# Kernel tuning notes

Measured on AMD Instinct MI355X. Metric: run time of the kernel, lower is better.

The kernel has to match this reference:

```python
import jax, jax.numpy as jnp
import numpy as np

N = 10000
E = 330000
B = 8
F_IN = 128
UNITS = 32
H1 = 4  # gat1 heads, concat -> 128
H2 = 1  # gat2 heads, average/no-concat -> 32


def setup_inputs() -> dict:
    key = jax.random.key(0)
    ks = jax.random.split(key, 12)
    x = jax.random.normal(ks[0], (B, N, F_IN), dtype=jnp.float32)
    # edges: random src/dst plus self loops appended (as in build())
    src = jax.random.randint(ks[1], (E,), 0, N, dtype=jnp.int32)
    dst = jax.random.randint(ks[2], (E,), 0, N, dtype=jnp.int32)
    loops = jnp.arange(N, dtype=jnp.int32)
    edge_src = jnp.concatenate([src, loops])
    edge_dst = jnp.concatenate([dst, loops])
    s = 0.05
    # GAT layer 1: F_IN -> UNITS per head, H1 heads
    W1 = jax.random.normal(ks[3], (F_IN, H1, UNITS), dtype=jnp.float32) * s
    a1_src = jax.random.normal(ks[4], (H1, UNITS), dtype=jnp.float32) * s
    a1_dst = jax.random.normal(ks[5], (H1, UNITS), dtype=jnp.float32) * s
    b1 = jnp.zeros((H1 * UNITS,), dtype=jnp.float32)
    # GAT layer 2: H1*UNITS -> UNITS, 1 head
    W2 = jax.random.normal(ks[6], (H1 * UNITS, H2, UNITS), dtype=jnp.float32) * s
    a2_src = jax.random.normal(ks[7], (H2, UNITS), dtype=jnp.float32) * s
    a2_dst = jax.random.normal(ks[8], (H2, UNITS), dtype=jnp.float32) * s
    b2 = jnp.zeros((UNITS,), dtype=jnp.float32)
    return {"x": x, "edge_src": edge_src, "edge_dst": edge_dst,
            "W1": W1, "a1_src": a1_src, "a1_dst": a1_dst, "b1": b1,
            "W2": W2, "a2_src": a2_src, "a2_dst": a2_dst, "b2": b2}


def gat_conv(x, edge_src, edge_dst, W, a_src, a_dst, b, concat):
    # x: [B, N, F]; W: [F, H, U]
    Bn, Nn, _ = x.shape
    H, U = W.shape[1], W.shape[2]
    h = jnp.einsum('bnf,fhu->bnhu', x, W)  # [B,N,H,U]
    # per-node attention logits split into src/dst parts (GATv1 style)
    e_src = jnp.einsum('bnhu,hu->bnh', h, a_src)  # [B,N,H]
    e_dst = jnp.einsum('bnhu,hu->bnh', h, a_dst)
    # gather along edges; edge e: src -> dst, aggregate at dst
    logits = e_src[:, edge_src, :] + e_dst[:, edge_dst, :]  # [B,E,H]
    logits = jax.nn.leaky_relu(logits, 0.2)
    # segment softmax over incoming edges of each dst node
    seg_max = jax.ops.segment_max(jnp.moveaxis(logits, 1, 0), edge_dst,
                                  num_segments=Nn)  # [N,B,H]
    seg_max = jnp.where(jnp.isfinite(seg_max), seg_max, 0.0)
    expv = jnp.exp(jnp.moveaxis(logits, 1, 0) - seg_max[edge_dst])  # [E,B,H]
    denom = jax.ops.segment_sum(expv, edge_dst, num_segments=Nn)  # [N,B,H]
    alpha = expv / (denom[edge_dst] + 1e-9)  # [E,B,H]
    # weighted scatter-add of source features
    msg = jnp.moveaxis(h, 1, 0)[edge_src] * alpha[..., None]  # [E,B,H,U]
    out = jax.ops.segment_sum(msg, edge_dst, num_segments=Nn)  # [N,B,H,U]
    out = jnp.moveaxis(out, 0, 1)  # [B,N,H,U]
    if concat:
        out = out.reshape(Bn, Nn, H * U)
    else:
        out = out.mean(axis=2)
    return out + b


def reference(x, edge_src, edge_dst, W1, a1_src, a1_dst, b1, W2, a2_src, a2_dst, b2):
    h1 = gat_conv(x, edge_src, edge_dst, W1, a1_src, a1_dst, b1, concat=True)
    h1 = jax.nn.relu(h1)
    out = gat_conv(h1, edge_src, edge_dst, W2, a2_src, a2_dst, b2, concat=False)
    return out
```

## Files before the change

kernel.cpp:

```cpp
#include <hip/hip_runtime.h>
#include <hip/hip_fp16.h>

#define N_NODES 10000
#define BATCH 8
#define FIN 128
#define UNITS 32
#define NH1 4
#define MAXDEG 128

#define WAVE_FENCE() asm volatile("s_waitcnt lgkmcnt(0)" ::: "memory")

#define FMA_MIX_LO(acc, u, a) \
    asm("v_fma_mix_f32 %0, %1, %2, %0 op_sel:[0,0,0] op_sel_hi:[1,0,0]" \
        : "+v"(acc) : "v"(u), "v"(a))
#define FMA_MIX_HI(acc, u, a) \
    asm("v_fma_mix_f32 %0, %1, %2, %0 op_sel:[1,0,0] op_sel_hi:[1,0,0]" \
        : "+v"(acc) : "v"(u), "v"(a))

typedef _Float16 half8 __attribute__((ext_vector_type(8)));
typedef float f32x4 __attribute__((ext_vector_type(4)));

__global__ void prep_kernel(const float* __restrict__ W1, const float* __restrict__ a1s,
                            const float* __restrict__ a1d, const float* __restrict__ W2,
                            const float* __restrict__ a2s, const float* __restrict__ a2d,
                            __half* __restrict__ Wt1, __half* __restrict__ Wt2) {
    int t = blockIdx.x * blockDim.x + threadIdx.x;
    const int N1 = 144 * 128;
    if (t < N1) {
        int c = t >> 7, k = t & 127;
        float v = 0.f;
        if (c < 128) v = W1[k * 128 + c];
        else if (c < 132) {
            int h = c - 128;
            for (int u = 0; u < 32; ++u) v += W1[k * 128 + h * 32 + u] * a1s[h * 32 + u];
        } else if (c < 136) {
            int h = c - 132;
            for (int u = 0; u < 32; ++u) v += W1[k * 128 + h * 32 + u] * a1d[h * 32 + u];
        }
        Wt1[t] = __float2half(v);
    } else if (t < N1 + 48 * 128) {
        int q = t - N1;
        int c = q >> 7, k = q & 127;
        float v = 0.f;
        if (c < 32) v = W2[k * 32 + c];
        else if (c == 32) { for (int u = 0; u < 32; ++u) v += W2[k * 32 + u] * a2s[u]; }
        else if (c == 33) { for (int u = 0; u < 32; ++u) v += W2[k * 32 + u] * a2d[u]; }
        Wt2[q] = __float2half(v);
    }
}

template<typename XT, int NTILES, int HTILES, int ES>
__global__ __launch_bounds__(256)
void gemm_mfma(const XT* __restrict__ X, const __half* __restrict__ Wt,
               __half* __restrict__ Hout, float* __restrict__ es,
               float* __restrict__ ed, int rows) {
    constexpr int K = 128;
    constexpr int HCOLS = HTILES * 16;
    constexpr int PAD = 136;
    __shared__ _Float16 Wl[NTILES * 16][PAD];
    const int tid = threadIdx.x;
    for (int idx = tid; idx < NTILES * 16 * K / 8; idx += 256) {
        int r = idx >> 4, kq = idx & 15;
        *(half8*)&Wl[r][kq * 8] = *(const half8*)(Wt + r * K + kq * 8);
    }
    __syncthreads();
    const int w = tid >> 6, lane = tid & 63;
    const int row16 = blockIdx.x * 64 + w * 16;
    const int arow = row16 + (lane & 15);
    const int cl = lane & 15;
    f32x4 acc[NTILES] = {};
    #pragma unroll
    for (int kb = 0; kb < 4; ++kb) {
        int kbase = kb * 32 + ((lane >> 4) << 3);
        half8 a;
        if constexpr (sizeof(XT) == 4) {
            const float* xp = (const float*)X + (size_t)arow * K + kbase;
            float4 v0 = *(const float4*)xp;
            float4 v1 = *(const float4*)(xp + 4);
            a[0] = v0.x; a[1] = v0.y; a[2] = v0.z; a[3] = v0.w;
            a[4] = v1.x; a[5] = v1.y; a[6] = v1.z; a[7] = v1.w;
        } else {
            a = *(const half8*)((const _Float16*)X + (size_t)arow * K + kbase);
        }
        #pragma unroll
        for (int t = 0; t < NTILES; ++t) {
            half8 b = *(const half8*)&Wl[t * 16 + cl][kbase];
            acc[t] = __builtin_amdgcn_mfma_f32_16x16x32_f16(a, b, acc[t], 0, 0, 0);
        }
    }
    const int rbase = row16 + ((lane >> 4) << 2);
    #pragma unroll
    for (int t = 0; t < HTILES; ++t) {
        #pragma unroll
        for (int i = 0; i < 4; ++i)
            Hout[(size_t)(rbase + i) * HCOLS + t * 16 + cl] = __float2half(acc[t][i]);
    }
    {
        f32x4 lg = acc[HTILES];
        if (cl < ES) {
            #pragma unroll
            for (int i = 0; i < 4; ++i) es[(size_t)(rbase + i) * ES + cl] = lg[i];
        } else if (cl < 2 * ES) {
            #pragma unroll
            for (int i = 0; i < 4; ++i) ed[(size_t)(rbase + i) * ES + (cl - ES)] = lg[i];
        }
    }
}

__global__ void build_kernel(const int* __restrict__ esrc, const int* __restrict__ edst,
                             int* __restrict__ deg, int* __restrict__ colPad, int E) {
    int e = blockIdx.x * blockDim.x + threadIdx.x;
    if (e >= E) return;
    int d = edst[e];
    int pos = atomicAdd(&deg[d], 1);
    colPad[(d << 7) + pos] = esrc[e];
}

__global__ __launch_bounds__(512)
void agg1_kernel(const int* __restrict__ deg, const int* __restrict__ colPad,
                 const float* __restrict__ es, const float* __restrict__ ed,
                 const __half* __restrict__ Hf, const float* __restrict__ bias,
                 __half* __restrict__ outH) {
    __shared__ float evS[8][MAXDEG][4];
    __shared__ int colS[8][MAXDEG];
    int blk = blockIdx.x;
    int b = blk & 7;
    int grp = blk >> 3;
    int w = threadIdx.x >> 6;
    int d = grp * 8 + w;
    int lane = threadIdx.x & 63;
    int eg = lane >> 4;
    int c8 = lane & 15;
    int head = c8 >> 2;
    int n = deg[d];
    const int* colp = colPad + (d << 7);
    size_t brow = (size_t)b * N_NODES;
    size_t drow = brow + d;
    float4 ed4 = ((const float4*)ed)[drow];
    float dx = 0.f, dy = 0.f, dz = 0.f, dw = 0.f;
    #pragma unroll
    for (int rep = 0; rep < 2; ++rep) {
        int i = lane + rep * 64;
        if (i < n) {
            int s = colp[i];
            colS[w][i] = s;
            float4 e4 = ((const float4*)es)[brow + s];
            float l, a0, a1, a2, a3;
            l = e4.x + ed4.x; l = l > 0.f ? l : 0.2f * l; a0 = __expf(l); dx += a0;
            l = e4.y + ed4.y; l = l > 0.f ? l : 0.2f * l; a1 = __expf(l); dy += a1;
            l = e4.z + ed4.z; l = l > 0.f ? l : 0.2f * l; a2 = __expf(l); dz += a2;
            l = e4.w + ed4.w; l = l > 0.f ? l : 0.2f * l; a3 = __expf(l); dw += a3;
            *(float4*)&evS[w][i][0] = make_float4(a0, a1, a2, a3);
        }
    }
    WAVE_FENCE();
    float acc[8] = {};
    const __half* hbase = Hf + (brow << 7) + (c8 << 3);
    int n16 = n & ~15;
    for (int t = 0; t < n16; t += 16) {
        int t0 = t + eg, t1 = t0 + 4, t2 = t0 + 8, t3 = t0 + 12;
        float a0 = evS[w][t0][head], a1 = evS[w][t1][head];
        float a2 = evS[w][t2][head], a3 = evS[w][t3][head];
        int s0 = colS[w][t0], s1 = colS[w][t1], s2 = colS[w][t2], s3 = colS[w][t3];
        float4 r0 = *(const float4*)(hbase + ((size_t)s0 << 7));
        float4 r1 = *(const float4*)(hbase + ((size_t)s1 << 7));
        float4 r2 = *(const float4*)(hbase + ((size_t)s2 << 7));
        float4 r3 = *(const float4*)(hbase + ((size_t)s3 << 7));
        const unsigned* u0 = (const unsigned*)&r0;
        const unsigned* u1 = (const unsigned*)&r1;
        const unsigned* u2 = (const unsigned*)&r2;
        const unsigned* u3 = (const unsigned*)&r3;
        #pragma unroll
        for (int j = 0; j < 4; ++j) {
            FMA_MIX_LO(acc[2 * j],     u0[j], a0);
            FMA_MIX_HI(acc[2 * j + 1], u0[j], a0);
        }
        #pragma unroll
        for (int j = 0; j < 4; ++j) {
            FMA_MIX_LO(acc[2 * j],     u1[j], a1);
            FMA_MIX_HI(acc[2 * j + 1], u1[j], a1);
        }
        #pragma unroll
        for (int j = 0; j < 4; ++j) {
            FMA_MIX_LO(acc[2 * j],     u2[j], a2);
            FMA_MIX_HI(acc[2 * j + 1], u2[j], a2);
        }
        #pragma unroll
        for (int j = 0; j < 4; ++j) {
            FMA_MIX_LO(acc[2 * j],     u3[j], a3);
            FMA_MIX_HI(acc[2 * j + 1], u3[j], a3);
        }
    }
    for (int t = n16; t < n; t += 4) {
        int myt = t + eg;
        int tt = myt < n ? myt : 0;
        float a = evS[w][tt][head]; if (myt >= n) a = 0.f;
        int s = colS[w][tt];
        float4 r = *(const float4*)(hbase + ((size_t)s << 7));
        const unsigned* u = (const unsigned*)&r;
        #pragma unroll
        for (int j = 0; j < 4; ++j) {
            FMA_MIX_LO(acc[2 * j],     u[j], a);
            FMA_MIX_HI(acc[2 * j + 1], u[j], a);
        }
    }
    #pragma unroll
    for (int off = 32; off; off >>= 1) {
        dx += __shfl_xor(dx, off);
        dy += __shfl_xor(dy, off);
        dz += __shfl_xor(dz, off);
        dw += __shfl_xor(dw, off);
    }
    float ix = 1.f / (dx + 1e-9f);
    float iy = 1.f / (dy + 1e-9f);
    float iz = 1.f / (dz + 1e-9f);
    float iw = 1.f / (dw + 1e-9f);
    float inv = (head & 2) ? ((head & 1) ? iw : iz) : ((head & 1) ? iy : ix);
    #pragma unroll
    for (int j = 0; j < 8; ++j) {
        acc[j] += __shfl_xor(acc[j], 16);
        acc[j] += __shfl_xor(acc[j], 32);
    }
    if (eg == 0) {
        float4 b0 = *(const float4*)(bias + 8 * c8);
        float4 b1 = *(const float4*)(bias + 8 * c8 + 4);
        float vals[8];
        vals[0] = fmaxf(acc[0] * inv + b0.x, 0.f);
        vals[1] = fmaxf(acc[1] * inv + b0.y, 0.f);
        vals[2] = fmaxf(acc[2] * inv + b0.z, 0.f);
        vals[3] = fmaxf(acc[3] * inv + b0.w, 0.f);
        vals[4] = fmaxf(acc[4] * inv + b1.x, 0.f);
        vals[5] = fmaxf(acc[5] * inv + b1.y, 0.f);
        vals[6] = fmaxf(acc[6] * inv + b1.z, 0.f);
        vals[7] = fmaxf(acc[7] * inv + b1.w, 0.f);
        __half2 o[4];
        #pragma unroll
        for (int j = 0; j < 4; ++j) o[j] = __floats2half2_rn(vals[2 * j], vals[2 * j + 1]);
        *(float4*)(outH + drow * 128 + c8 * 8) = *(float4*)o;
    }
}

__global__ __launch_bounds__(512)
void agg2_kernel(const int* __restrict__ deg, const int* __restrict__ colPad,
                 const float* __restrict__ es, const float* __restrict__ ed,
                 const __half* __restrict__ Hf, const float* __restrict__ bias,
                 float* __restrict__ outF) {
    __shared__ float evS[8][MAXDEG];
    __shared__ int colS[8][MAXDEG];
    int blk = blockIdx.x;
    int b = blk & 7;
    int grp = blk >> 3;
    int w = threadIdx.x >> 6;
    int d = grp * 8 + w;
    int lane = threadIdx.x & 63;
    int eg = lane >> 2;
    int c8 = lane & 3;
    int n = deg[d];
    const int* colp = colPad + (d << 7);
    size_t brow = (size_t)b * N_NODES;
    size_t drow = brow + d;
    float edv = ed[drow];
    float den = 0.f;
    #pragma unroll
    for (int rep = 0; rep < 2; ++rep) {
        int i = lane + rep * 64;
        if (i < n) {
            int s = colp[i];
            colS[w][i] = s;
            float l = es[brow + s] + edv;
            l = l > 0.f ? l : 0.2f * l;
            float ev = __expf(l);
            den += ev;
            evS[w][i] = ev;
        }
    }
    WAVE_FENCE();
    float acc[8] = {};
    const __half* hbase = Hf + (brow << 5) + (c8 << 3);
    int n32 = n & ~31;
    for (int t = 0; t < n32; t += 32) {
        int t0 = t + eg, t1 = t0 + 16;
        float a0 = evS[w][t0];
        float a1 = evS[w][t1];
        int s0 = colS[w][t0];
        int s1 = colS[w][t1];
        float4 r0 = *(const float4*)(hbase + ((size_t)s0 << 5));
        float4 r1 = *(const float4*)(hbase + ((size_t)s1 << 5));
        const unsigned* u0 = (const unsigned*)&r0;
        const unsigned* u1 = (const unsigned*)&r1;
        #pragma unroll
        for (int j = 0; j < 4; ++j) {
            FMA_MIX_LO(acc[2 * j],     u0[j], a0);
            FMA_MIX_HI(acc[2 * j + 1], u0[j], a0);
        }
        #pragma unroll
        for (int j = 0; j < 4; ++j) {
            FMA_MIX_LO(acc[2 * j],     u1[j], a1);
            FMA_MIX_HI(acc[2 * j + 1], u1[j], a1);
        }
    }
    for (int t = n32; t < n; t += 16) {
        int myt = t + eg;
        int tt = myt < n ? myt : 0;
        float a = evS[w][tt]; if (myt >= n) a = 0.f;
        int s = colS[w][tt];
        float4 r = *(const float4*)(hbase + ((size_t)s << 5));
        const unsigned* u = (const unsigned*)&r;
        #pragma unroll
        for (int j = 0; j < 4; ++j) {
            FMA_MIX_LO(acc[2 * j],     u[j], a);
            FMA_MIX_HI(acc[2 * j + 1], u[j], a);
        }
    }
    #pragma unroll
    for (int off = 32; off; off >>= 1) den += __shfl_xor(den, off);
    float inv = 1.f / (den + 1e-9f);
    #pragma unroll
    for (int j = 0; j < 8; ++j) {
        acc[j] += __shfl_xor(acc[j], 4);
        acc[j] += __shfl_xor(acc[j], 8);
        acc[j] += __shfl_xor(acc[j], 16);
        acc[j] += __shfl_xor(acc[j], 32);
    }
    if (eg == 0) {
        float4 b0 = *(const float4*)(bias + 8 * c8);
        float4 b1 = *(const float4*)(bias + 8 * c8 + 4);
        float4 o0, o1;
        o0.x = acc[0] * inv + b0.x;
        o0.y = acc[1] * inv + b0.y;
        o0.z = acc[2] * inv + b0.z;
        o0.w = acc[3] * inv + b0.w;
        o1.x = acc[4] * inv + b1.x;
        o1.y = acc[5] * inv + b1.y;
        o1.z = acc[6] * inv + b1.z;
        o1.w = acc[7] * inv + b1.w;
        float* op = outF + drow * 32 + 8 * c8;
        *(float4*)op = o0;
        *(float4*)(op + 4) = o1;
    }
}

extern "C" void kernel_launch(void* const* d_in, const int* in_sizes, int n_in,
                              void* d_out, int out_size, void* d_ws, size_t ws_size,
                              hipStream_t stream) {
    const float* x    = (const float*)d_in[0];
    const int*   esrc = (const int*)d_in[1];
    const int*   edst = (const int*)d_in[2];
    const float* W1   = (const float*)d_in[3];
    const float* a1s  = (const float*)d_in[4];
    const float* a1d  = (const float*)d_in[5];
    const float* b1   = (const float*)d_in[6];
    const float* W2   = (const float*)d_in[7];
    const float* a2s  = (const float*)d_in[8];
    const float* a2d  = (const float*)d_in[9];
    const float* b2   = (const float*)d_in[10];
    float* out = (float*)d_out;
    const int E = in_sizes[1];
    const int rows = BATCH * N_NODES;

    float* wsf = (float*)d_ws;
    __half* h1h   = (__half*)wsf;
    float*  e1s   = wsf + (size_t)rows * 64;
    float*  e1d   = e1s + (size_t)rows * 4;
    __half* out1h = (__half*)(e1d + (size_t)rows * 4);
    int* deg      = (int*)((float*)out1h + (size_t)rows * 64);
    int* colPad   = deg + N_NODES;
    __half* Wt1   = (__half*)(colPad + N_NODES * 128);
    __half* Wt2   = Wt1 + 144 * 128;
    __half* h2h = h1h;
    float*  e2s = e1s;
    float*  e2d = e1s + rows;

    const int TPB = 256;

    hipMemsetAsync(deg, 0, N_NODES * sizeof(int), stream);
    prep_kernel<<<(144 * 128 + 48 * 128 + TPB - 1) / TPB, TPB, 0, stream>>>(
        W1, a1s, a1d, W2, a2s, a2d, Wt1, Wt2);
    build_kernel<<<(E + TPB - 1) / TPB, TPB, 0, stream>>>(esrc, edst, deg, colPad, E);

    gemm_mfma<float, 9, 8, 4><<<rows / 64, 256, 0, stream>>>(
        x, Wt1, h1h, e1s, e1d, rows);
    agg1_kernel<<<(N_NODES / 8) * BATCH, 512, 0, stream>>>(deg, colPad, e1s, e1d, h1h, b1, out1h);

    gemm_mfma<__half, 3, 2, 1><<<rows / 64, 256, 0, stream>>>(
        out1h, Wt2, h2h, e2s, e2d, rows);
    agg2_kernel<<<(N_NODES / 8) * BATCH, 512, 0, stream>>>(deg, colPad, e2s, e2d, h2h, b2, out);
}
```

Before: 154.6 us.

## Fuse build and prep kernels, compute layer-2 logits in agg1 epilogue

Merges the edge-list build and the weight-prep kernels into a single launch. The layer-2 attention logit projections (W2·a2s, W2·a2d) are now applied in fp32 inside the agg1 epilogue, so the second GEMM drops its extra MFMA tile. Neighbour indices are pre-shifted into byte offsets and stored in shared memory, which removes per-edge shift arithmetic in both aggregation kernels. In exchange, agg1 does extra dot products and shuffles, and the layer-2 logits come from fp32 values instead of the fp16 GEMM path.

```diff
diff --git a/kernel.cpp b/kernel.cpp
--- a/kernel.cpp
+++ b/kernel.cpp
@@ -20,13 +20,27 @@
 typedef _Float16 half8 __attribute__((ext_vector_type(8)));
 typedef float f32x4 __attribute__((ext_vector_type(4)));
 
-__global__ void prep_kernel(const float* __restrict__ W1, const float* __restrict__ a1s,
-                            const float* __restrict__ a1d, const float* __restrict__ W2,
-                            const float* __restrict__ a2s, const float* __restrict__ a2d,
-                            __half* __restrict__ Wt1, __half* __restrict__ Wt2) {
-    int t = blockIdx.x * blockDim.x + threadIdx.x;
-    const int N1 = 144 * 128;
-    if (t < N1) {
+__global__ void build_prep_kernel(const int* __restrict__ esrc, const int* __restrict__ edst,
+                                  int* __restrict__ deg, int* __restrict__ colPad, int E, int EB,
+                                  const float* __restrict__ W1, const float* __restrict__ a1s,
+                                  const float* __restrict__ a1d, const float* __restrict__ W2,
+                                  const float* __restrict__ a2s, const float* __restrict__ a2d,
+                                  __half* __restrict__ Wt1, __half* __restrict__ Wt2,
+                                  float* __restrict__ wa2) {
+    int blk = blockIdx.x;
+    if (blk < EB) {
+        int e = blk * 256 + threadIdx.x;
+        if (e < E) {
+            int d = edst[e];
+            int pos = atomicAdd(&deg[d], 1);
+            colPad[(d << 7) + pos] = esrc[e];
+        }
+        return;
+    }
+    int t = (blk - EB) * 256 + threadIdx.x;
+    const int NP1 = 144 * 128;
+    const int NP2 = 48 * 128;
+    if (t < NP1) {
         int c = t >> 7, k = t & 127;
         float v = 0.f;
         if (c < 128) v = W1[k * 128 + c];
@@ -38,14 +52,18 @@
             for (int u = 0; u < 32; ++u) v += W1[k * 128 + h * 32 + u] * a1d[h * 32 + u];
         }
         Wt1[t] = __float2half(v);
-    } else if (t < N1 + 48 * 128) {
-        int q = t - N1;
+    } else if (t < NP1 + NP2) {
+        int q = t - NP1;
         int c = q >> 7, k = q & 127;
+        float v = (c < 32) ? W2[k * 32 + c] : 0.f;
+        Wt2[q] = __float2half(v);
+    } else if (t < NP1 + NP2 + 256) {
+        int c = t - NP1 - NP2;
+        int k = c & 127;
+        const float* a = (c < 128) ? a2s : a2d;
         float v = 0.f;
-        if (c < 32) v = W2[k * 32 + c];
-        else if (c == 32) { for (int u = 0; u < 32; ++u) v += W2[k * 32 + u] * a2s[u]; }
-        else if (c == 33) { for (int u = 0; u < 32; ++u) v += W2[k * 32 + u] * a2d[u]; }
-        Wt2[q] = __float2half(v);
+        for (int u = 0; u < 32; ++u) v += W2[k * 32 + u] * a[u];
+        wa2[c] = v;
     }
 }
 
@@ -95,7 +113,7 @@
         for (int i = 0; i < 4; ++i)
             Hout[(size_t)(rbase + i) * HCOLS + t * 16 + cl] = __float2half(acc[t][i]);
     }
-    {
+    if constexpr (ES > 0) {
         f32x4 lg = acc[HTILES];
         if (cl < ES) {
             #pragma unroll
@@ -107,20 +125,12 @@
     }
 }
 
-__global__ void build_kernel(const int* __restrict__ esrc, const int* __restrict__ edst,
-                             int* __restrict__ deg, int* __restrict__ colPad, int E) {
-    int e = blockIdx.x * blockDim.x + threadIdx.x;
-    if (e >= E) return;
-    int d = edst[e];
-    int pos = atomicAdd(&deg[d], 1);
-    colPad[(d << 7) + pos] = esrc[e];
-}
-
 __global__ __launch_bounds__(512)
 void agg1_kernel(const int* __restrict__ deg, const int* __restrict__ colPad,
                  const float* __restrict__ es, const float* __restrict__ ed,
                  const __half* __restrict__ Hf, const float* __restrict__ bias,
-                 __half* __restrict__ outH) {
+                 const float* __restrict__ wa2, __half* __restrict__ outH,
+                 float* __restrict__ e2s, float* __restrict__ e2d) {
     __shared__ float evS[8][MAXDEG][4];
     __shared__ int colS[8][MAXDEG];
     int blk = blockIdx.x;
@@ -143,7 +153,7 @@
         int i = lane + rep * 64;
         if (i < n) {
             int s = colp[i];
-            colS[w][i] = s;
+            colS[w][i] = s << 8;
             float4 e4 = ((const float4*)es)[brow + s];
             float l, a0, a1, a2, a3;
             l = e4.x + ed4.x; l = l > 0.f ? l : 0.2f * l; a0 = __expf(l); dx += a0;
@@ -155,17 +165,17 @@
     }
     WAVE_FENCE();
     float acc[8] = {};
-    const __half* hbase = Hf + (brow << 7) + (c8 << 3);
+    const char* hbase = (const char*)Hf + (brow << 8) + (c8 << 4);
     int n16 = n & ~15;
     for (int t = 0; t < n16; t += 16) {
         int t0 = t + eg, t1 = t0 + 4, t2 = t0 + 8, t3 = t0 + 12;
         float a0 = evS[w][t0][head], a1 = evS[w][t1][head];
         float a2 = evS[w][t2][head], a3 = evS[w][t3][head];
-        int s0 = colS[w][t0], s1 = colS[w][t1], s2 = colS[w][t2], s3 = colS[w][t3];
-        float4 r0 = *(const float4*)(hbase + ((size_t)s0 << 7));
-        float4 r1 = *(const float4*)(hbase + ((size_t)s1 << 7));
-        float4 r2 = *(const float4*)(hbase + ((size_t)s2 << 7));
-        float4 r3 = *(const float4*)(hbase + ((size_t)s3 << 7));
+        int o0 = colS[w][t0], o1 = colS[w][t1], o2 = colS[w][t2], o3 = colS[w][t3];
+        float4 r0 = *(const float4*)(hbase + o0);
+        float4 r1 = *(const float4*)(hbase + o1);
+        float4 r2 = *(const float4*)(hbase + o2);
+        float4 r3 = *(const float4*)(hbase + o3);
         const unsigned* u0 = (const unsigned*)&r0;
         const unsigned* u1 = (const unsigned*)&r1;
         const unsigned* u2 = (const unsigned*)&r2;
@@ -195,8 +205,8 @@
         int myt = t + eg;
         int tt = myt < n ? myt : 0;
         float a = evS[w][tt][head]; if (myt >= n) a = 0.f;
-        int s = colS[w][tt];
-        float4 r = *(const float4*)(hbase + ((size_t)s << 7));
+        int o = colS[w][tt];
+        float4 r = *(const float4*)(hbase + o);
         const unsigned* u = (const unsigned*)&r;
         #pragma unroll
         for (int j = 0; j < 4; ++j) {
@@ -237,6 +247,20 @@
         #pragma unroll
         for (int j = 0; j < 4; ++j) o[j] = __floats2half2_rn(vals[2 * j], vals[2 * j + 1]);
         *(float4*)(outH + drow * 128 + c8 * 8) = *(float4*)o;
+        const float* w2s = wa2 + 8 * c8;
+        const float* w2d = wa2 + 128 + 8 * c8;
+        float es2 = vals[0] * w2s[0] + vals[1] * w2s[1] + vals[2] * w2s[2] + vals[3] * w2s[3]
+                  + vals[4] * w2s[4] + vals[5] * w2s[5] + vals[6] * w2s[6] + vals[7] * w2s[7];
+        float ed2 = vals[0] * w2d[0] + vals[1] * w2d[1] + vals[2] * w2d[2] + vals[3] * w2d[3]
+                  + vals[4] * w2d[4] + vals[5] * w2d[5] + vals[6] * w2d[6] + vals[7] * w2d[7];
+        es2 += __shfl_xor(es2, 1); es2 += __shfl_xor(es2, 2);
+        es2 += __shfl_xor(es2, 4); es2 += __shfl_xor(es2, 8);
+        ed2 += __shfl_xor(ed2, 1); ed2 += __shfl_xor(ed2, 2);
+        ed2 += __shfl_xor(ed2, 4); ed2 += __shfl_xor(ed2, 8);
+        if (c8 == 0) {
+            e2s[drow] = es2;
+            e2d[drow] = ed2;
+        }
     }
 }
 
@@ -266,7 +290,7 @@
         int i = lane + rep * 64;
         if (i < n) {
             int s = colp[i];
-            colS[w][i] = s;
+            colS[w][i] = s << 6;
             float l = es[brow + s] + edv;
             l = l > 0.f ? l : 0.2f * l;
             float ev = __expf(l);
@@ -276,16 +300,16 @@
     }
     WAVE_FENCE();
     float acc[8] = {};
-    const __half* hbase = Hf + (brow << 5) + (c8 << 3);
+    const char* hbase = (const char*)Hf + (brow << 6) + (c8 << 4);
     int n32 = n & ~31;
     for (int t = 0; t < n32; t += 32) {
         int t0 = t + eg, t1 = t0 + 16;
         float a0 = evS[w][t0];
         float a1 = evS[w][t1];
-        int s0 = colS[w][t0];
-        int s1 = colS[w][t1];
-        float4 r0 = *(const float4*)(hbase + ((size_t)s0 << 5));
-        float4 r1 = *(const float4*)(hbase + ((size_t)s1 << 5));
+        int o0 = colS[w][t0];
+        int o1 = colS[w][t1];
+        float4 r0 = *(const float4*)(hbase + o0);
+        float4 r1 = *(const float4*)(hbase + o1);
         const unsigned* u0 = (const unsigned*)&r0;
         const unsigned* u1 = (const unsigned*)&r1;
         #pragma unroll
@@ -303,8 +327,8 @@
         int myt = t + eg;
         int tt = myt < n ? myt : 0;
         float a = evS[w][tt]; if (myt >= n) a = 0.f;
-        int s = colS[w][tt];
-        float4 r = *(const float4*)(hbase + ((size_t)s << 5));
+        int o = colS[w][tt];
+        float4 r = *(const float4*)(hbase + o);
         const unsigned* u = (const unsigned*)&r;
         #pragma unroll
         for (int j = 0; j < 4; ++j) {
@@ -367,22 +391,26 @@
     int* colPad   = deg + N_NODES;
     __half* Wt1   = (__half*)(colPad + N_NODES * 128);
     __half* Wt2   = Wt1 + 144 * 128;
-    __half* h2h = h1h;
-    float*  e2s = e1s;
-    float*  e2d = e1s + rows;
+    float* wa2    = (float*)(Wt2 + 48 * 128);
+    float* e2s    = wa2 + 256;
+    float* e2d    = e2s + rows;
+    __half* h2h   = h1h;
 
     const int TPB = 256;
+    const int EB = (E + TPB - 1) / TPB;
+    const int PREPB = (144 * 128 + 48 * 128 + 256 + TPB - 1) / TPB;
 
     hipMemsetAsync(deg, 0, N_NODES * sizeof(int), stream);
-    prep_kernel<<<(144 * 128 + 48 * 128 + TPB - 1) / TPB, TPB, 0, stream>>>(
-        W1, a1s, a1d, W2, a2s, a2d, Wt1, Wt2);
-    build_kernel<<<(E + TPB - 1) / TPB, TPB, 0, stream>>>(esrc, edst, deg, colPad, E);
+    build_prep_kernel<<<EB + PREPB, TPB, 0, stream>>>(
+        esrc, edst, deg, colPad, E, EB, W1, a1s, a1d, W2, a2s, a2d, Wt1, Wt2, wa2);
 
     gemm_mfma<float, 9, 8, 4><<<rows / 64, 256, 0, stream>>>(
         x, Wt1, h1h, e1s, e1d, rows);
-    agg1_kernel<<<(N_NODES / 8) * BATCH, 512, 0, stream>>>(deg, colPad, e1s, e1d, h1h, b1, out1h);
-
-    gemm_mfma<__half, 3, 2, 1><<<rows / 64, 256, 0, stream>>>(
-        out1h, Wt2, h2h, e2s, e2d, rows);
-    agg2_kernel<<<(N_NODES / 8) * BATCH, 512, 0, stream>>>(deg, colPad, e2s, e2d, h2h, b2, out);
+    agg1_kernel<<<(N_NODES / 8) * BATCH, 512, 0, stream>>>(
+        deg, colPad, e1s, e1d, h1h, b1, wa2, out1h, e2s, e2d);
+
+    gemm_mfma<__half, 2, 2, 0><<<rows / 64, 256, 0, stream>>>(
+        out1h, Wt2, h2h, nullptr, nullptr, rows);
+    agg2_kernel<<<(N_NODES / 8) * BATCH, 512, 0, stream>>>(
+        deg, colPad, e2s, e2d, h2h, b2, out);
 }
```

Measured after the change: 157.6 us. No clear change (+2.0%).
